# Performance work log

Measured on AMD Instinct MI355X. Metric: run time of the kernel, lower is better.

Reference implementation:

```python
import jax, jax.numpy as jnp
import numpy as np

NUM_USERS = 200000
NUM_PRODUCTS = 100000
N_NODES = NUM_USERS + NUM_PRODUCTS
N_EDGES = 1000000
USER_FDIM = 128
PROD_FDIM = 128
EDIM = 64


def setup_inputs() -> dict:
    key = jax.random.key(0)
    ks = jax.random.split(key, 16)
    s = 0.02
    inp = {
        "edge_index": jnp.stack([
            jax.random.randint(ks[0], (N_EDGES,), 0, NUM_USERS, dtype=jnp.int32).astype(jnp.int64),
            jax.random.randint(ks[1], (N_EDGES,), 0, NUM_PRODUCTS, dtype=jnp.int32).astype(jnp.int64),
        ], axis=0),
        "user_features": jax.random.normal(ks[2], (NUM_USERS, USER_FDIM), jnp.float32),
        "product_features": jax.random.normal(ks[3], (NUM_PRODUCTS, PROD_FDIM), jnp.float32),
        "user_emb": jax.random.normal(ks[4], (NUM_USERS, EDIM), jnp.float32) * s,
        "product_emb": jax.random.normal(ks[5], (NUM_PRODUCTS, EDIM), jnp.float32) * s,
        "W_uf": jax.random.normal(ks[6], (USER_FDIM, EDIM), jnp.float32) * s,
        "b_uf": jnp.zeros((EDIM,), jnp.float32),
        "W_pf": jax.random.normal(ks[7], (PROD_FDIM, EDIM), jnp.float32) * s,
        "b_pf": jnp.zeros((EDIM,), jnp.float32),
        "conv1_W": jax.random.normal(ks[8], (EDIM, EDIM), jnp.float32) * s,
        "conv1_b": jnp.zeros((EDIM,), jnp.float32),
        "conv2_W": jax.random.normal(ks[9], (EDIM, EDIM), jnp.float32) * s,
        "conv2_b": jnp.zeros((EDIM,), jnp.float32),
        "pred_W1": jax.random.normal(ks[10], (2 * EDIM, EDIM), jnp.float32) * s,
        "pred_b1": jnp.zeros((EDIM,), jnp.float32),
        "pred_W2": jax.random.normal(ks[11], (EDIM, 1), jnp.float32) * s,
        "pred_b2": jnp.zeros((1,), jnp.float32),
    }
    return inp


def _gcn_conv(x, W, b, row, col, n_nodes):
    # PyG GCNConv: h = x W; out[col] += deg^-1/2[row] * deg^-1/2[col] * h[row]; + b
    h = x @ W
    deg = jax.ops.segment_sum(jnp.ones_like(col, dtype=x.dtype), col, num_segments=n_nodes)
    dis = jnp.where(deg > 0, jax.lax.rsqrt(jnp.maximum(deg, 1.0)), 0.0)
    norm = dis[row] * dis[col]                     # [E_total]
    msgs = h[row] * norm[:, None]                  # gather + edge weight
    out = jax.ops.segment_sum(msgs, col, num_segments=n_nodes)  # scatter-add
    return out + b


def reference(edge_index, user_features, product_features, user_emb, product_emb,
              W_uf, b_uf, W_pf, b_pf, conv1_W, conv1_b, conv2_W, conv2_b,
              pred_W1, pred_b1, pred_W2, pred_b2):
    user_idx = edge_index[0]
    prod_idx = edge_index[1]

    user_x = user_features @ W_uf + b_uf + user_emb          # [Nu, D]
    prod_x = product_features @ W_pf + b_pf + product_emb    # [Np, D]
    x = jnp.concatenate([user_x, prod_x], axis=0)            # [N, D]

    # symmetrized edges + self-loops (GCNConv default add_self_loops=True)
    ar = jnp.arange(N_NODES, dtype=edge_index.dtype)
    row = jnp.concatenate([user_idx, prod_idx, ar])
    col = jnp.concatenate([prod_idx, user_idx, ar])

    x = jax.nn.relu(_gcn_conv(x, conv1_W, conv1_b, row, col, N_NODES))
    # dropout p=0.2 is identity in eval mode
    x = _gcn_conv(x, conv2_W, conv2_b, row, col, N_NODES)

    user_e = x[:NUM_USERS][user_idx]                          # [E, D]
    prod_e = x[NUM_USERS:][prod_idx]                          # [E, D]
    pair = jnp.concatenate([user_e, prod_e], axis=1)          # [E, 2D]
    h = jax.nn.relu(pair @ pred_W1 + pred_b1)
    logits = h @ pred_W2 + pred_b2                            # [E, 1]
    preds = jax.nn.sigmoid(logits).squeeze(-1) * 5.0
    return preds
```

## Files before the change

### kernel.cpp

```cpp
#include <hip/hip_runtime.h>
#include <math.h>

#define NUM_USERS 200000
#define NUM_PRODUCTS 100000
#define N_NODES 300000
#define N_EDGES 1000000
#define EDIM 64
#define FDIM 128
#define CAP 40
#define LDST 72
#define NT_U 12500
#define NT_P 6250
#define NT_ALL 18750
#define ZERO_BLK 1173
#define NBUK 80
#define BNODES 2500
#define BINCAP 49152
#define CSR_REP 4
#define XC1_BLOCKS 1024
#define XC1_WAVES (XC1_BLOCKS * 4)
#define XC1_UW 2731

typedef __attribute__((ext_vector_type(8))) short short8;
typedef __attribute__((ext_vector_type(4))) float f32x4;

static __device__ inline short f2bf(float f) {
    unsigned int u = __float_as_uint(f);
    unsigned int r = (u + 0x7FFFu + ((u >> 16) & 1u)) >> 16;
    return (short)r;
}
static __device__ inline float bf2f(unsigned short s) {
    return __uint_as_float(((unsigned int)s) << 16);
}
static __device__ inline float disf(int c) {
    return rsqrtf(1.0f + (float)c);
}

__global__ void k_setup(int* __restrict__ cnt,
                        const float* __restrict__ W_uf, const float* __restrict__ W_pf,
                        const float* __restrict__ c1, const float* __restrict__ c2,
                        const float* __restrict__ W1, short* __restrict__ wts) {
    int b = blockIdx.x;
    if (b < ZERO_BLK) {
        int i = b * 256 + threadIdx.x;
        if (i < 300032 + NBUK) cnt[i] = 0;
        return;
    }
    int gid = (b - ZERO_BLK) * 256 + threadIdx.x;
    if (gid >= 32768) return;
    if (gid < 8192) {
        int n = gid >> 7, k = gid & 127;
        wts[gid] = f2bf(W_uf[k * 64 + n]);
    } else if (gid < 16384) {
        int i = gid - 8192; int n = i >> 7, k = i & 127;
        wts[gid] = f2bf(W_pf[k * 64 + n]);
    } else if (gid < 20480) {
        int i = gid - 16384; int n = i >> 6, k = i & 63;
        wts[gid] = f2bf(c1[k * 64 + n]);
    } else if (gid < 24576) {
        int i = gid - 20480; int n = i >> 6, k = i & 63;
        wts[gid] = f2bf(c2[k * 64 + n]);
    } else {
        int i = gid - 24576; int n = i >> 7, k = i & 127;
        wts[gid] = f2bf(W1[k * 64 + n]);
    }
}

__global__ __launch_bounds__(256) void k_bin(
    const int* __restrict__ ei, int* __restrict__ gcnt, int* __restrict__ gbin) {
    __shared__ int lcnt[NBUK];
    __shared__ int lbase[NBUK];
    int tid = threadIdx.x;
    if (tid < NBUK) lcnt[tid] = 0;
    __syncthreads();
    int e0 = (blockIdx.x * 256 + tid) * 4;
    bool act = e0 < N_EDGES;
    int d[8], s[8], rk[8], bk[8];
    if (act) {
        int4 uu = *(const int4*)(ei + e0);
        int4 pp = *(const int4*)(ei + N_EDGES + e0);
        d[0] = pp.x; s[0] = uu.x;  d[1] = uu.x; s[1] = pp.x;
        d[2] = pp.y; s[2] = uu.y;  d[3] = uu.y; s[3] = pp.y;
        d[4] = pp.z; s[4] = uu.z;  d[5] = uu.z; s[5] = pp.z;
        d[6] = pp.w; s[6] = uu.w;  d[7] = uu.w; s[7] = pp.w;
#pragma unroll
        for (int j = 0; j < 8; ++j) {
            bk[j] = d[j] / BNODES;
            rk[j] = atomicAdd(&lcnt[bk[j]], 1);
        }
    }
    __syncthreads();
    if (tid < NBUK) lbase[tid] = atomicAdd(&gcnt[tid], lcnt[tid]);
    __syncthreads();
    if (act) {
#pragma unroll
        for (int j = 0; j < 8; ++j) {
            int pos = lbase[bk[j]] + rk[j];
            if (pos < BINCAP)
                *(int2*)(gbin + ((size_t)bk[j] * BINCAP + pos) * 2) = make_int2(d[j], s[j]);
        }
    }
}

__global__ __launch_bounds__(256) void k_csr(
    const int* __restrict__ gcnt, const int* __restrict__ gbin,
    int* __restrict__ cnt, int* __restrict__ adj) {
    int i = blockIdx.x;
    int xcd = i & 7, k = i >> 3;
    int bucket = (k % (NBUK / 8)) * 8 + xcd;
    int rep = k / (NBUK / 8);
    int n = gcnt[bucket];
    const int* bb = gbin + (size_t)bucket * BINCAP * 2;
    const int stride = CSR_REP * 256;
    int idx = rep * 256 + threadIdx.x;
    for (; idx + 3 * stride < n; idx += 4 * stride) {
        int2 e0 = *(const int2*)(bb + (size_t)(idx)*2);
        int2 e1 = *(const int2*)(bb + (size_t)(idx + stride) * 2);
        int2 e2 = *(const int2*)(bb + (size_t)(idx + 2 * stride) * 2);
        int2 e3 = *(const int2*)(bb + (size_t)(idx + 3 * stride) * 2);
        int s0 = atomicAdd(&cnt[e0.x], 1);
        int s1 = atomicAdd(&cnt[e1.x], 1);
        int s2 = atomicAdd(&cnt[e2.x], 1);
        int s3 = atomicAdd(&cnt[e3.x], 1);
        adj[(size_t)e0.x * CAP + s0] = e0.y;
        adj[(size_t)e1.x * CAP + s1] = e1.y;
        adj[(size_t)e2.x * CAP + s2] = e2.y;
        adj[(size_t)e3.x * CAP + s3] = e3.y;
    }
    for (; idx < n; idx += stride) {
        int2 e = *(const int2*)(bb + (size_t)idx * 2);
        int s = atomicAdd(&cnt[e.x], 1);
        adj[(size_t)e.x * CAP + s] = e.y;
    }
}

#define XC1_LOAD(S, MT) do {                                                         \
    int mb_ = (MT) * 16;                                                             \
    const float* ar_ = feat + (size_t)(mb_ + ln) * FDIM + quad * 8;                  \
    _Pragma("unroll")                                                                \
    for (int kk_ = 0; kk_ < 4; ++kk_) {                                              \
        fl##S[kk_] = *(const float4*)(ar_ + kk_ * 32);                               \
        fh##S[kk_] = *(const float4*)(ar_ + kk_ * 32 + 4);                           \
    }                                                                                \
    _Pragma("unroll")                                                                \
    for (int r_ = 0; r_ < 4; ++r_)                                                   \
        _Pragma("unroll")                                                            \
        for (int t_ = 0; t_ < 4; ++t_)                                               \
            ev##S[r_][t_] = emb[(size_t)(mb_ + quad * 4 + r_) * EDIM + t_ * 16 + ln];\
    _Pragma("unroll")                                                                \
    for (int r_ = 0; r_ < 4; ++r_)                                                   \
        cd##S[r_] = cnt[node_off + mb_ + quad * 4 + r_];                             \
} while (0)

#define XC1_COMPUTE(S, MT) do {                                                      \
    int mb_ = (MT) * 16;                                                             \
    f32x4 acc_[4] = {{0.f,0.f,0.f,0.f},{0.f,0.f,0.f,0.f},{0.f,0.f,0.f,0.f},{0.f,0.f,0.f,0.f}}; \
    _Pragma("unroll")                                                                \
    for (int kk_ = 0; kk_ < 4; ++kk_) {                                              \
        short8 Af_;                                                                  \
        Af_[0] = f2bf(fl##S[kk_].x); Af_[1] = f2bf(fl##S[kk_].y);                    \
        Af_[2] = f2bf(fl##S[kk_].z); Af_[3] = f2bf(fl##S[kk_].w);                    \
        Af_[4] = f2bf(fh##S[kk_].x); Af_[5] = f2bf(fh##S[kk_].y);                    \
        Af_[6] = f2bf(fh##S[kk_].z); Af_[7] = f2bf(fh##S[kk_].w);                    \
        _Pragma("unroll")                                                            \
        for (int t_ = 0; t_ < 4; ++t_)                                               \
            acc_[t_] = __builtin_amdgcn_mfma_f32_16x16x32_bf16(Af_, Bx[t_][kk_], acc_[t_], 0, 0, 0); \
    }                                                                                \
    _Pragma("unroll")                                                                \
    for (int r_ = 0; r_ < 4; ++r_)                                                   \
        _Pragma("unroll")                                                            \
        for (int t_ = 0; t_ < 4; ++t_) {                                             \
            float v_ = acc_[t_][r_] + bv[t_] + ev##S[r_][t_];                        \
            lds[wave][(quad * 4 + r_) * LDST + t_ * 16 + ln] = (unsigned short)f2bf(v_); \
        }                                                                            \
    f32x4 acch_[4] = {{0.f,0.f,0.f,0.f},{0.f,0.f,0.f,0.f},{0.f,0.f,0.f,0.f},{0.f,0.f,0.f,0.f}}; \
    _Pragma("unroll")                                                                \
    for (int kk_ = 0; kk_ < 2; ++kk_) {                                              \
        short8 Af_ = *(const short8*)(&lds[wave][ln * LDST + kk_ * 32 + quad * 8]);  \
        _Pragma("unroll")                                                            \
        for (int t_ = 0; t_ < 4; ++t_)                                               \
            acch_[t_] = __builtin_amdgcn_mfma_f32_16x16x32_bf16(Af_, Bc[t_][kk_], acch_[t_], 0, 0, 0); \
    }                                                                                \
    _Pragma("unroll")                                                                \
    for (int r_ = 0; r_ < 4; ++r_) {                                                 \
        float dv_ = disf(cd##S[r_]);                                                 \
        int node_ = mb_ + quad * 4 + r_;                                             \
        _Pragma("unroll")                                                            \
        for (int t_ = 0; t_ < 4; ++t_)                                               \
            h[(size_t)(node_off + node_) * EDIM + t_ * 16 + ln] =                    \
                (unsigned short)f2bf(dv_ * acch_[t_][r_]);                           \
    }                                                                                \
} while (0)

__global__ __launch_bounds__(256, 2) void k_xform_c1(
    const float* __restrict__ user_feat, const float* __restrict__ prod_feat,
    const short* __restrict__ wts,
    const float* __restrict__ b_uf, const float* __restrict__ b_pf,
    const float* __restrict__ user_emb, const float* __restrict__ prod_emb,
    const int* __restrict__ cnt, unsigned short* __restrict__ h) {
    __shared__ unsigned short lds[4][16 * LDST];
    int tid = threadIdx.x;
    int wave = tid >> 6;
    int lane = tid & 63, ln = lane & 15, quad = lane >> 4;
    int gw = blockIdx.x * 4 + wave;

    const float* feat; const short* WT; const float* b; const float* emb;
    int node_off, t0, tcnt, tstride;
    if (gw < XC1_UW) {
        feat = user_feat; WT = wts;        b = b_uf; emb = user_emb;
        node_off = 0;         t0 = gw;          tcnt = NT_U; tstride = XC1_UW;
    } else {
        feat = prod_feat; WT = wts + 8192; b = b_pf; emb = prod_emb;
        node_off = NUM_USERS; t0 = gw - XC1_UW; tcnt = NT_P; tstride = XC1_WAVES - XC1_UW;
    }
    if (t0 >= tcnt) return;
    const short* c1T = wts + 16384;

    short8 Bx[4][4];
#pragma unroll
    for (int t = 0; t < 4; ++t)
#pragma unroll
        for (int kk = 0; kk < 4; ++kk)
            Bx[t][kk] = *(const short8*)(WT + ((t * 16 + ln) * 128 + kk * 32 + quad * 8));
    short8 Bc[4][2];
#pragma unroll
    for (int t = 0; t < 4; ++t)
#pragma unroll
        for (int kk = 0; kk < 2; ++kk)
            Bc[t][kk] = *(const short8*)(c1T + ((t * 16 + ln) * 64 + kk * 32 + quad * 8));
    float bv[4];
#pragma unroll
    for (int t = 0; t < 4; ++t) bv[t] = b[t * 16 + ln];

    float4 flA[4], fhA[4], flB[4], fhB[4];
    float evA[4][4], evB[4][4];
    int cdA[4], cdB[4];

    int t = t0;
    XC1_LOAD(A, t);
    for (;;) {
        int tn = t + tstride;
        bool hasB = tn < tcnt;
        if (hasB) XC1_LOAD(B, tn);
        XC1_COMPUTE(A, t);
        if (!hasB) break;
        t = tn;
        tn = t + tstride;
        bool hasA = tn < tcnt;
        if (hasA) XC1_LOAD(A, tn);
        XC1_COMPUTE(B, t);
        if (!hasA) break;
        t = tn;
    }
}

__global__ __launch_bounds__(256) void k_gather_c2(
    const int* __restrict__ adj, const int* __restrict__ cnt,
    const unsigned short* __restrict__ h,
    const float* __restrict__ b1, const short* __restrict__ c2T,
    unsigned short* __restrict__ hout) {
    __shared__ unsigned short lds[4][16 * LDST];
    int tid = threadIdx.x;
    int wave = tid >> 6;
    int tile = blockIdx.x * 4 + wave;
    if (tile >= N_NODES / 16) return;
    int lane = tid & 63, ln = lane & 15, quad = lane >> 4;
    const unsigned int* hp = (const unsigned int*)h;

    short8 Bc[4][2];
#pragma unroll
    for (int t = 0; t < 4; ++t)
#pragma unroll
        for (int kk = 0; kk < 2; ++kk)
            Bc[t][kk] = *(const short8*)(c2T + ((t * 16 + ln) * 64 + kk * 32 + quad * 8));

    int mbase = tile * 16;
    float2 bb0 = ((const float2*)b1)[ln];
    float2 bb1 = ((const float2*)b1)[16 + ln];

#pragma unroll 1
    for (int it = 0; it < 4; ++it) {
        int d = mbase + it * 4 + quad;
        const unsigned int* hrow = hp + (size_t)d * 32;
        unsigned int s0 = hrow[ln], s1 = hrow[16 + ln];
        float a0 = bf2f((unsigned short)s0);
        float a1 = bf2f((unsigned short)(s0 >> 16));
        float a2 = bf2f((unsigned short)s1);
        float a3 = bf2f((unsigned short)(s1 >> 16));
        int cd = cnt[d];
        const int* ap = adj + (size_t)d * CAP;
        int i = 0;
        for (; i + 1 < cd; i += 2) {
            int r0 = ap[i], r1 = ap[i + 1];
            unsigned int p00 = hp[(size_t)r0 * 32 + ln];
            unsigned int p01 = hp[(size_t)r0 * 32 + 16 + ln];
            unsigned int p10 = hp[(size_t)r1 * 32 + ln];
            unsigned int p11 = hp[(size_t)r1 * 32 + 16 + ln];
            a0 += bf2f((unsigned short)p00) + bf2f((unsigned short)p10);
            a1 += bf2f((unsigned short)(p00 >> 16)) + bf2f((unsigned short)(p10 >> 16));
            a2 += bf2f((unsigned short)p01) + bf2f((unsigned short)p11);
            a3 += bf2f((unsigned short)(p01 >> 16)) + bf2f((unsigned short)(p11 >> 16));
        }
        if (i < cd) {
            int r0 = ap[i];
            unsigned int p00 = hp[(size_t)r0 * 32 + ln];
            unsigned int p01 = hp[(size_t)r0 * 32 + 16 + ln];
            a0 += bf2f((unsigned short)p00);
            a1 += bf2f((unsigned short)(p00 >> 16));
            a2 += bf2f((unsigned short)p01);
            a3 += bf2f((unsigned short)(p01 >> 16));
        }
        float dv = disf(cd);
        float v0 = fmaxf(fmaf(dv, a0, bb0.x), 0.f);
        float v1 = fmaxf(fmaf(dv, a1, bb0.y), 0.f);
        float v2 = fmaxf(fmaf(dv, a2, bb1.x), 0.f);
        float v3 = fmaxf(fmaf(dv, a3, bb1.y), 0.f);
        unsigned int* lrow = (unsigned int*)&lds[wave][(it * 4 + quad) * LDST];
        lrow[ln] = ((unsigned int)(unsigned short)f2bf(v1) << 16)
                 | (unsigned int)(unsigned short)f2bf(v0);
        lrow[16 + ln] = ((unsigned int)(unsigned short)f2bf(v3) << 16)
                      | (unsigned int)(unsigned short)f2bf(v2);
    }
    f32x4 acc[4] = {{0.f,0.f,0.f,0.f},{0.f,0.f,0.f,0.f},{0.f,0.f,0.f,0.f},{0.f,0.f,0.f,0.f}};
#pragma unroll
    for (int kk = 0; kk < 2; ++kk) {
        short8 Af = *(const short8*)(&lds[wave][ln * LDST + kk * 32 + quad * 8]);
#pragma unroll
        for (int t = 0; t < 4; ++t)
            acc[t] = __builtin_amdgcn_mfma_f32_16x16x32_bf16(Af, Bc[t][kk], acc[t], 0, 0, 0);
    }
    float disv[4];
#pragma unroll
    for (int r = 0; r < 4; ++r) disv[r] = disf(cnt[mbase + quad * 4 + r]);
#pragma unroll
    for (int r = 0; r < 4; ++r) {
        int node = mbase + quad * 4 + r;
#pragma unroll
        for (int t = 0; t < 4; ++t)
            hout[(size_t)node * EDIM + t * 16 + ln] = (unsigned short)f2bf(disv[r] * acc[t][r]);
    }
}

__global__ __launch_bounds__(256) void k_gather(
    const int* __restrict__ adj, const int* __restrict__ cnt,
    const unsigned short* __restrict__ h,
    const float* __restrict__ b, unsigned short* __restrict__ xout, int relu) {
    int d = blockIdx.x * 4 + (threadIdx.x >> 6);
    if (d >= N_NODES) return;
    int l = threadIdx.x & 63;
    int half = l >> 5, c2 = l & 31;
    const unsigned int* hp = (const unsigned int*)h;

    float ax = 0.f, ay = 0.f;
    if (half == 0) {
        unsigned int pr = hp[(size_t)d * 32 + c2];
        ax = bf2f((unsigned short)pr);
        ay = bf2f((unsigned short)(pr >> 16));
    }
    int c = cnt[d];
    const int* ap = adj + (size_t)d * CAP;
    int i = 0;
    for (; i + 3 < c; i += 4) {
        int s0 = ap[i + half];
        int s1 = ap[i + 2 + half];
        unsigned int p0 = hp[(size_t)s0 * 32 + c2];
        unsigned int p1 = hp[(size_t)s1 * 32 + c2];
        ax += bf2f((unsigned short)p0) + bf2f((unsigned short)p1);
        ay += bf2f((unsigned short)(p0 >> 16)) + bf2f((unsigned short)(p1 >> 16));
    }
    if (i + half < c) {
        unsigned int p0 = hp[(size_t)ap[i + half] * 32 + c2];
        ax += bf2f((unsigned short)p0);
        ay += bf2f((unsigned short)(p0 >> 16));
    }
    if (i + 2 + half < c) {
        unsigned int p0 = hp[(size_t)ap[i + 2 + half] * 32 + c2];
        ax += bf2f((unsigned short)p0);
        ay += bf2f((unsigned short)(p0 >> 16));
    }
    ax += __shfl_xor(ax, 32, 64);
    ay += __shfl_xor(ay, 32, 64);
    float dv = disf(c);
    float2 bb = ((const float2*)b)[c2];
    float v0 = fmaf(dv, ax, bb.x);
    float v1 = fmaf(dv, ay, bb.y);
    if (relu) { v0 = fmaxf(v0, 0.f); v1 = fmaxf(v1, 0.f); }
    if (half == 0) {
        unsigned int pk = ((unsigned int)(unsigned short)f2bf(v1) << 16)
                        | (unsigned int)(unsigned short)f2bf(v0);
        ((unsigned int*)xout)[(size_t)d * 32 + c2] = pk;
    }
}

__global__ __launch_bounds__(256) void k_pred_mfma(
    const int* __restrict__ ei, const unsigned short* __restrict__ x,
    const short* __restrict__ W1T, const float* __restrict__ b1,
    const float* __restrict__ W2, const float* __restrict__ b2,
    float* __restrict__ preds) {
    int tid = threadIdx.x;
    int wave = tid >> 6, lane = tid & 63;
    int ln = lane & 15, quad = lane >> 4;

    short8 Bf[4][4];
#pragma unroll
    for (int t = 0; t < 4; ++t)
#pragma unroll
        for (int kk = 0; kk < 4; ++kk)
            Bf[t][kk] = *(const short8*)(W1T + ((t * 16 + ln) * 128 + kk * 32 + quad * 8));

    float b1v[4], W2v[4];
#pragma unroll
    for (int t = 0; t < 4; ++t) {
        b1v[t] = b1[t * 16 + ln];
        W2v[t] = W2[t * 16 + ln];
    }
    float b2s = b2[0];

    const int n_tiles = N_EDGES / 16;
    int gw = blockIdx.x * 4 + wave;
    int nwaves = gridDim.x * 4;

    int cu = 0, cp = 0;
    if (gw < n_tiles) {
        cu = ei[gw * 16 + ln];
        cp = ei[N_EDGES + gw * 16 + ln] + NUM_USERS;
    }
    for (int tile = gw; tile < n_tiles; tile += nwaves) {
        int u = cu, p = cp;
        int nt = tile + nwaves;
        if (nt < n_tiles) {
            cu = ei[nt * 16 + ln];
            cp = ei[N_EDGES + nt * 16 + ln] + NUM_USERS;
        }
        short8 Af[4];
        Af[0] = *(const short8*)(x + (size_t)u * EDIM + quad * 8);
        Af[1] = *(const short8*)(x + (size_t)u * EDIM + 32 + quad * 8);
        Af[2] = *(const short8*)(x + (size_t)p * EDIM + quad * 8);
        Af[3] = *(const short8*)(x + (size_t)p * EDIM + 32 + quad * 8);

        f32x4 acc[4] = {{0.f,0.f,0.f,0.f},{0.f,0.f,0.f,0.f},{0.f,0.f,0.f,0.f},{0.f,0.f,0.f,0.f}};
#pragma unroll
        for (int kk = 0; kk < 4; ++kk)
#pragma unroll
            for (int t = 0; t < 4; ++t)
                acc[t] = __builtin_amdgcn_mfma_f32_16x16x32_bf16(Af[kk], Bf[t][kk], acc[t], 0, 0, 0);

        float out[4];
#pragma unroll
        for (int r = 0; r < 4; ++r) {
            float part = 0.f;
#pragma unroll
            for (int t = 0; t < 4; ++t) {
                float hv = fmaxf(acc[t][r] + b1v[t], 0.f);
                part = fmaf(hv, W2v[t], part);
            }
            part += __shfl_xor(part, 1, 64);
            part += __shfl_xor(part, 2, 64);
            part += __shfl_xor(part, 4, 64);
            part += __shfl_xor(part, 8, 64);
            out[r] = part;
        }
        if (ln == 0) {
            int ebase = tile * 16;
#pragma unroll
            for (int r = 0; r < 4; ++r) {
                float logit = out[r] + b2s;
                preds[ebase + quad * 4 + r] = 5.f / (1.f + expf(-logit));
            }
        }
    }
}

extern "C" void kernel_launch(void* const* d_in, const int* in_sizes, int n_in,
                              void* d_out, int out_size, void* d_ws, size_t ws_size,
                              hipStream_t stream) {
    const int*   ei        = (const int*)d_in[0];
    const float* user_feat = (const float*)d_in[1];
    const float* prod_feat = (const float*)d_in[2];
    const float* user_emb  = (const float*)d_in[3];
    const float* prod_emb  = (const float*)d_in[4];
    const float* W_uf      = (const float*)d_in[5];
    const float* b_uf      = (const float*)d_in[6];
    const float* W_pf      = (const float*)d_in[7];
    const float* b_pf      = (const float*)d_in[8];
    const float* conv1_W   = (const float*)d_in[9];
    const float* conv1_b   = (const float*)d_in[10];
    const float* conv2_W   = (const float*)d_in[11];
    const float* conv2_b   = (const float*)d_in[12];
    const float* pred_W1   = (const float*)d_in[13];
    const float* pred_b1   = (const float*)d_in[14];
    const float* pred_W2   = (const float*)d_in[15];
    const float* pred_b2   = (const float*)d_in[16];

    int* ws_i = (int*)d_ws;
    int*   cnt  = ws_i;
    int*   gcnt = ws_i + 300032;
    int*   adj  = ws_i + 600064;
    unsigned short* xbuf = (unsigned short*)(ws_i + 12601344);
    int*   gbin = ws_i + 12601344;
    unsigned short* hbuf = (unsigned short*)(ws_i + 22201344);
    short* wts = (short*)(ws_i + 31801344);
    float* preds = (float*)d_out;

    k_setup<<<ZERO_BLK + 128, 256, 0, stream>>>(cnt, W_uf, W_pf, conv1_W, conv2_W, pred_W1, wts);
    k_bin<<<(N_EDGES / 4 + 255) / 256, 256, 0, stream>>>(ei, gcnt, gbin);
    k_csr<<<NBUK * CSR_REP, 256, 0, stream>>>(gcnt, gbin, cnt, adj);

    k_xform_c1<<<XC1_BLOCKS, 256, 0, stream>>>(user_feat, prod_feat, wts,
                                               b_uf, b_pf, user_emb, prod_emb,
                                               cnt, hbuf);

    k_gather_c2<<<(18750 + 3) / 4, 256, 0, stream>>>(adj, cnt, hbuf, conv1_b,
                                                     wts + 20480, xbuf);
    k_gather<<<N_NODES / 4, 256, 0, stream>>>(adj, cnt, xbuf, conv2_b, hbuf, 0);

    k_pred_mfma<<<2048, 256, 0, stream>>>(ei, hbuf, wts + 24576, pred_b1, pred_W2, pred_b2, preds);
}
```

Baseline: 670.6 us.

## Build CSR adjacency per bucket in shared memory and write out coalesced

Buckets shrink to 320 nodes so each k_csr block owns one bucket, counts slots with LDS atomics and stages the adjacency rows in shared memory, then writes cnt and adj with coalesced int4 stores. This removes global atomics on cnt and scattered 4-byte adj writes. The cost is about 51KB of LDS per block, which limits occupancy. k_bin now uses 625 buckets, so more LDS counters and more global bucket atomics per block.

```diff
diff --git a/kernel.cpp b/kernel.cpp
--- a/kernel.cpp
+++ b/kernel.cpp
@@ -12,11 +12,10 @@
 #define NT_U 12500
 #define NT_P 6250
 #define NT_ALL 18750
-#define ZERO_BLK 1173
-#define NBUK 80
-#define BNODES 2500
-#define BINCAP 49152
-#define CSR_REP 4
+#define NBUK 625
+#define BNODES 320
+#define BINCAP 6144
+#define ZERO_BLK 1175
 #define XC1_BLOCKS 1024
 #define XC1_WAVES (XC1_BLOCKS * 4)
 #define XC1_UW 2731
@@ -71,7 +70,7 @@
     __shared__ int lcnt[NBUK];
     __shared__ int lbase[NBUK];
     int tid = threadIdx.x;
-    if (tid < NBUK) lcnt[tid] = 0;
+    for (int i = tid; i < NBUK; i += 256) lcnt[i] = 0;
     __syncthreads();
     int e0 = (blockIdx.x * 256 + tid) * 4;
     bool act = e0 < N_EDGES;
@@ -90,7 +89,7 @@
         }
     }
     __syncthreads();
-    if (tid < NBUK) lbase[tid] = atomicAdd(&gcnt[tid], lcnt[tid]);
+    for (int i = tid; i < NBUK; i += 256) lbase[i] = atomicAdd(&gcnt[i], lcnt[i]);
     __syncthreads();
     if (act) {
 #pragma unroll
@@ -105,33 +104,28 @@
 __global__ __launch_bounds__(256) void k_csr(
     const int* __restrict__ gcnt, const int* __restrict__ gbin,
     int* __restrict__ cnt, int* __restrict__ adj) {
-    int i = blockIdx.x;
-    int xcd = i & 7, k = i >> 3;
-    int bucket = (k % (NBUK / 8)) * 8 + xcd;
-    int rep = k / (NBUK / 8);
+    __shared__ int lcnt[BNODES];
+    __shared__ __align__(16) int stage[BNODES * CAP];
+    int bucket = blockIdx.x;
+    int base = bucket * BNODES;
+    int tid = threadIdx.x;
+    for (int i = tid; i < BNODES; i += 256) lcnt[i] = 0;
+    __syncthreads();
     int n = gcnt[bucket];
+    if (n > BINCAP) n = BINCAP;
     const int* bb = gbin + (size_t)bucket * BINCAP * 2;
-    const int stride = CSR_REP * 256;
-    int idx = rep * 256 + threadIdx.x;
-    for (; idx + 3 * stride < n; idx += 4 * stride) {
-        int2 e0 = *(const int2*)(bb + (size_t)(idx)*2);
-        int2 e1 = *(const int2*)(bb + (size_t)(idx + stride) * 2);
-        int2 e2 = *(const int2*)(bb + (size_t)(idx + 2 * stride) * 2);
-        int2 e3 = *(const int2*)(bb + (size_t)(idx + 3 * stride) * 2);
-        int s0 = atomicAdd(&cnt[e0.x], 1);
-        int s1 = atomicAdd(&cnt[e1.x], 1);
-        int s2 = atomicAdd(&cnt[e2.x], 1);
-        int s3 = atomicAdd(&cnt[e3.x], 1);
-        adj[(size_t)e0.x * CAP + s0] = e0.y;
-        adj[(size_t)e1.x * CAP + s1] = e1.y;
-        adj[(size_t)e2.x * CAP + s2] = e2.y;
-        adj[(size_t)e3.x * CAP + s3] = e3.y;
-    }
-    for (; idx < n; idx += stride) {
+    for (int idx = tid; idx < n; idx += 256) {
         int2 e = *(const int2*)(bb + (size_t)idx * 2);
-        int s = atomicAdd(&cnt[e.x], 1);
-        adj[(size_t)e.x * CAP + s] = e.y;
-    }
+        int ln = e.x - base;
+        int s = atomicAdd(&lcnt[ln], 1);
+        stage[ln * CAP + s] = e.y;
+    }
+    __syncthreads();
+    for (int i = tid; i < BNODES; i += 256) cnt[base + i] = lcnt[i];
+    int4* dst = (int4*)(adj + (size_t)base * CAP);
+    const int4* src = (const int4*)stage;
+#pragma unroll 4
+    for (int i = tid; i < BNODES * CAP / 4; i += 256) dst[i] = src[i];
 }
 
 #define XC1_LOAD(S, MT) do {                                                         \
@@ -504,7 +498,7 @@
 
     k_setup<<<ZERO_BLK + 128, 256, 0, stream>>>(cnt, W_uf, W_pf, conv1_W, conv2_W, pred_W1, wts);
     k_bin<<<(N_EDGES / 4 + 255) / 256, 256, 0, stream>>>(ei, gcnt, gbin);
-    k_csr<<<NBUK * CSR_REP, 256, 0, stream>>>(gcnt, gbin, cnt, adj);
+    k_csr<<<NBUK, 256, 0, stream>>>(gcnt, gbin, cnt, adj);
 
     k_xform_c1<<<XC1_BLOCKS, 256, 0, stream>>>(user_feat, prod_feat, wts,
                                                b_uf, b_pf, user_emb, prod_emb,
```

New measurement: 582.6 us. 13.1% less time.
